# Optimization experiments

Measured on AMD Instinct MI355X. Metric: run time of the kernel, lower is better.

The kernel has to match this reference:

```python
import jax, jax.numpy as jnp
import numpy as np


def setup_inputs() -> dict:
    key = jax.random.key(0)
    k1, k2, k3 = jax.random.split(key, 3)
    B, S, H = 32, 2048, 1024
    lstm_output = jax.random.normal(k1, (B, S, H), dtype=jnp.float32)
    final_hidden = jax.random.normal(k2, (B, H), dtype=jnp.float32)
    # nn.Linear(2H, 1): weight [1, 2H], bias [1]
    W = jax.random.normal(k3, (1, 2 * H), dtype=jnp.float32) * (1.0 / np.sqrt(2 * H))
    b = jnp.zeros((1,), dtype=jnp.float32)
    return {"lstm_output": lstm_output, "final_hidden": final_hidden, "W": W, "b": b}


def reference(lstm_output, final_hidden, W, b):
    # Equivalent to cat([lstm_output, repeat(final_hidden)]) @ W.T + b,
    # but split W to avoid materializing the [B, S, 2H] concat.
    H = lstm_output.shape[-1]
    w1 = W[0, :H]   # applies to lstm_output
    w2 = W[0, H:]   # applies to final_hidden
    # scores: [B, S]
    scores = jnp.einsum('bsh,h->bs', lstm_output, w1) \
           + (final_hidden @ w2)[:, None] + b[0]
    attn_weights = jax.nn.softmax(scores, axis=1)              # [B, S]
    context_vector = jnp.einsum('bs,bsh->bh', attn_weights, lstm_output)
    return context_vector, attn_weights
```

## Files before the change

### kernel.cpp

```cpp
#include <hip/hip_runtime.h>


#define B_ 32
#define S_ 2048
#define H_ 1024
#define ROWS 32
#define WAVES_PER_BATCH (S_ / ROWS)
#define NWAVE (B_ * WAVES_PER_BATCH)
#define NBLK (NWAVE / 4)

__global__ __launch_bounds__(256) void fused_pass(
    const float* __restrict__ lstm, const float* __restrict__ W,
    float* __restrict__ scores, float* __restrict__ part, float* __restrict__ lpart)
{
    const int tid  = threadIdx.x;
    const int wave = tid >> 6;
    const int lane = tid & 63;
    const int gw   = blockIdx.x * 4 + wave;
    const int b    = gw >> 6;
    const int s0   = (gw & 63) * ROWS;

    float4 w[4];
#pragma unroll
    for (int q = 0; q < 4; ++q)
        w[q] = *(const float4*)(W + q * 256 + lane * 4);

    float4 acc[4];
#pragma unroll
    for (int q = 0; q < 4; ++q) acc[q] = make_float4(0.f, 0.f, 0.f, 0.f);
    float l = 0.f;

    const float* base = lstm + ((size_t)b * S_ + s0) * H_ + lane * 4;

    float4 v[4];
#pragma unroll
    for (int q = 0; q < 4; ++q) v[q] = *(const float4*)(base + q * 256);

#pragma unroll
    for (int r = 0; r < ROWS; ++r) {
        float4 nv[4];
        if (r + 1 < ROWS) {
            const float* nb = base + (size_t)(r + 1) * H_;
#pragma unroll
            for (int q = 0; q < 4; ++q) nv[q] = *(const float4*)(nb + q * 256);
        }
        float d = v[0].x * w[0].x + v[0].y * w[0].y + v[0].z * w[0].z + v[0].w * w[0].w;
#pragma unroll
        for (int q = 1; q < 4; ++q)
            d += v[q].x * w[q].x + v[q].y * w[q].y + v[q].z * w[q].z + v[q].w * w[q].w;
#pragma unroll
        for (int off = 32; off >= 1; off >>= 1)
            d += __shfl_xor(d, off, 64);
        if (lane == 0) scores[(size_t)b * S_ + s0 + r] = d;
        const float e = __expf(d);
        l += e;
#pragma unroll
        for (int q = 0; q < 4; ++q) {
            acc[q].x += e * v[q].x; acc[q].y += e * v[q].y;
            acc[q].z += e * v[q].z; acc[q].w += e * v[q].w;
        }
        if (r + 1 < ROWS) {
#pragma unroll
            for (int q = 0; q < 4; ++q) v[q] = nv[q];
        }
    }

    float* pp = part + (size_t)gw * H_ + lane * 4;
#pragma unroll
    for (int q = 0; q < 4; ++q) *(float4*)(pp + q * 256) = acc[q];
    if (lane == 0) lpart[gw] = l;
}

__global__ __launch_bounds__(128) void combine_k(
    const float* __restrict__ part, const float* __restrict__ lpart,
    float* __restrict__ ctx_out, float* __restrict__ Lws)
{
    const int b = blockIdx.x;
    const int h = blockIdx.y * 128 + threadIdx.x;
    float L = 0.f;
#pragma unroll
    for (int j = 0; j < WAVES_PER_BATCH; ++j)
        L += lpart[b * WAVES_PER_BATCH + j];
    float sum = 0.f;
#pragma unroll 8
    for (int j = 0; j < WAVES_PER_BATCH; ++j)
        sum += part[(size_t)(b * WAVES_PER_BATCH + j) * H_ + h];
    ctx_out[(size_t)b * H_ + h] = sum / L;
    if (blockIdx.y == 0 && threadIdx.x == 0) Lws[b] = L;
}

__global__ __launch_bounds__(256) void attn_k(
    const float* __restrict__ scores, const float* __restrict__ Lws,
    float* __restrict__ attn_out)
{
    const int i = blockIdx.x * 256 + threadIdx.x;
    const int b = i >> 9;
    const float invL = 1.0f / Lws[b];
    const float4 sc = ((const float4*)scores)[i];
    float4 o;
    o.x = __expf(sc.x) * invL;
    o.y = __expf(sc.y) * invL;
    o.z = __expf(sc.z) * invL;
    o.w = __expf(sc.w) * invL;
    ((float4*)attn_out)[i] = o;
}

extern "C" void kernel_launch(void* const* d_in, const int* in_sizes, int n_in,
                              void* d_out, int out_size, void* d_ws, size_t ws_size,
                              hipStream_t stream)
{
    const float* lstm = (const float*)d_in[0];
    const float* W    = (const float*)d_in[2];

    float* out  = (float*)d_out;
    float* ctx  = out;
    float* attn = out + B_ * H_;

    float* ws     = (float*)d_ws;
    float* scores = ws;
    float* part   = ws + (size_t)B_ * S_;
    float* lpart  = part + (size_t)NWAVE * H_;
    float* Lws    = lpart + NWAVE;

    fused_pass<<<NBLK, 256, 0, stream>>>(lstm, W, scores, part, lpart);
    combine_k<<<dim3(B_, H_ / 128), 128, 0, stream>>>(part, lpart, ctx, Lws);
    attn_k<<<(B_ * S_) / (4 * 256), 256, 0, stream>>>(scores, Lws, attn);
}
```

Baseline: 403.8 us.

## Batch four-row loads per wave, halve rows per wave, store exp scores

The main pass now loads four rows of lstm_output at once and does their dot products, shuffle reductions and accumulation together. Before, each wave kept only one row of loads in flight ahead of the compute. The number of rows per wave drops from 32 to 16, which doubles the wave count, and exp(score) is written directly so attn_k only has to scale it. The aim is more outstanding memory requests to hide load latency, at the cost of a partial-sum buffer twice as large that combine_k must write and read. combine_k also moves to 256-thread blocks.

```diff
diff --git a/kernel.cpp b/kernel.cpp
--- a/kernel.cpp
+++ b/kernel.cpp
@@ -4,21 +4,21 @@
 #define B_ 32
 #define S_ 2048
 #define H_ 1024
-#define ROWS 32
+#define ROWS 16
 #define WAVES_PER_BATCH (S_ / ROWS)
 #define NWAVE (B_ * WAVES_PER_BATCH)
 #define NBLK (NWAVE / 4)
 
 __global__ __launch_bounds__(256) void fused_pass(
     const float* __restrict__ lstm, const float* __restrict__ W,
-    float* __restrict__ scores, float* __restrict__ part, float* __restrict__ lpart)
+    float* __restrict__ esc, float* __restrict__ part, float* __restrict__ lpart)
 {
     const int tid  = threadIdx.x;
     const int wave = tid >> 6;
     const int lane = tid & 63;
     const int gw   = blockIdx.x * 4 + wave;
-    const int b    = gw >> 6;
-    const int s0   = (gw & 63) * ROWS;
+    const int b    = gw >> 7;
+    const int s0   = (gw & 127) * ROWS;
 
     float4 w[4];
 #pragma unroll
@@ -32,36 +32,49 @@
 
     const float* base = lstm + ((size_t)b * S_ + s0) * H_ + lane * 4;
 
-    float4 v[4];
 #pragma unroll
-    for (int q = 0; q < 4; ++q) v[q] = *(const float4*)(base + q * 256);
+    for (int t = 0; t < ROWS / 4; ++t) {
+        const float* rb = base + (size_t)(t * 4) * H_;
+        float4 v[4][4];
+#pragma unroll
+        for (int r = 0; r < 4; ++r)
+#pragma unroll
+            for (int q = 0; q < 4; ++q)
+                v[r][q] = *(const float4*)(rb + (size_t)r * H_ + q * 256);
 
+        float d[4];
 #pragma unroll
-    for (int r = 0; r < ROWS; ++r) {
-        float4 nv[4];
-        if (r + 1 < ROWS) {
-            const float* nb = base + (size_t)(r + 1) * H_;
+        for (int r = 0; r < 4; ++r) {
+            float s = v[r][0].x * w[0].x + v[r][0].y * w[0].y
+                    + v[r][0].z * w[0].z + v[r][0].w * w[0].w;
 #pragma unroll
-            for (int q = 0; q < 4; ++q) nv[q] = *(const float4*)(nb + q * 256);
+            for (int q = 1; q < 4; ++q)
+                s += v[r][q].x * w[q].x + v[r][q].y * w[q].y
+                   + v[r][q].z * w[q].z + v[r][q].w * w[q].w;
+            d[r] = s;
         }
-        float d = v[0].x * w[0].x + v[0].y * w[0].y + v[0].z * w[0].z + v[0].w * w[0].w;
 #pragma unroll
-        for (int q = 1; q < 4; ++q)
-            d += v[q].x * w[q].x + v[q].y * w[q].y + v[q].z * w[q].z + v[q].w * w[q].w;
+        for (int off = 32; off >= 1; off >>= 1) {
 #pragma unroll
-        for (int off = 32; off >= 1; off >>= 1)
-            d += __shfl_xor(d, off, 64);
-        if (lane == 0) scores[(size_t)b * S_ + s0 + r] = d;
-        const float e = __expf(d);
-        l += e;
+            for (int r = 0; r < 4; ++r)
+                d[r] += __shfl_xor(d[r], off, 64);
+        }
+        float e[4];
 #pragma unroll
-        for (int q = 0; q < 4; ++q) {
-            acc[q].x += e * v[q].x; acc[q].y += e * v[q].y;
-            acc[q].z += e * v[q].z; acc[q].w += e * v[q].w;
-        }
-        if (r + 1 < ROWS) {
+        for (int r = 0; r < 4; ++r) e[r] = __expf(d[r]);
+        if (lane == 0)
+            *(float4*)(esc + (size_t)b * S_ + s0 + t * 4) =
+                make_float4(e[0], e[1], e[2], e[3]);
+        l += (e[0] + e[1]) + (e[2] + e[3]);
 #pragma unroll
-            for (int q = 0; q < 4; ++q) v[q] = nv[q];
+        for (int r = 0; r < 4; ++r) {
+#pragma unroll
+            for (int q = 0; q < 4; ++q) {
+                acc[q].x = fmaf(e[r], v[r][q].x, acc[q].x);
+                acc[q].y = fmaf(e[r], v[r][q].y, acc[q].y);
+                acc[q].z = fmaf(e[r], v[r][q].z, acc[q].z);
+                acc[q].w = fmaf(e[r], v[r][q].w, acc[q].w);
+            }
         }
     }
 
@@ -71,14 +84,14 @@
     if (lane == 0) lpart[gw] = l;
 }
 
-__global__ __launch_bounds__(128) void combine_k(
+__global__ __launch_bounds__(256) void combine_k(
     const float* __restrict__ part, const float* __restrict__ lpart,
     float* __restrict__ ctx_out, float* __restrict__ Lws)
 {
     const int b = blockIdx.x;
-    const int h = blockIdx.y * 128 + threadIdx.x;
+    const int h = blockIdx.y * 256 + threadIdx.x;
     float L = 0.f;
-#pragma unroll
+#pragma unroll 16
     for (int j = 0; j < WAVES_PER_BATCH; ++j)
         L += lpart[b * WAVES_PER_BATCH + j];
     float sum = 0.f;
@@ -90,18 +103,15 @@
 }
 
 __global__ __launch_bounds__(256) void attn_k(
-    const float* __restrict__ scores, const float* __restrict__ Lws,
+    const float* __restrict__ esc, const float* __restrict__ Lws,
     float* __restrict__ attn_out)
 {
     const int i = blockIdx.x * 256 + threadIdx.x;
     const int b = i >> 9;
     const float invL = 1.0f / Lws[b];
-    const float4 sc = ((const float4*)scores)[i];
+    const float4 e = ((const float4*)esc)[i];
     float4 o;
-    o.x = __expf(sc.x) * invL;
-    o.y = __expf(sc.y) * invL;
-    o.z = __expf(sc.z) * invL;
-    o.w = __expf(sc.w) * invL;
+    o.x = e.x * invL; o.y = e.y * invL; o.z = e.z * invL; o.w = e.w * invL;
     ((float4*)attn_out)[i] = o;
 }
 
@@ -116,13 +126,13 @@
     float* ctx  = out;
     float* attn = out + B_ * H_;
 
-    float* ws     = (float*)d_ws;
-    float* scores = ws;
-    float* part   = ws + (size_t)B_ * S_;
-    float* lpart  = part + (size_t)NWAVE * H_;
-    float* Lws    = lpart + NWAVE;
+    float* ws    = (float*)d_ws;
+    float* esc   = ws;
+    float* part  = ws + (size_t)B_ * S_;
+    float* lpart = part + (size_t)NWAVE * H_;
+    float* Lws   = lpart + NWAVE;
 
-    fused_pass<<<NBLK, 256, 0, stream>>>(lstm, W, scores, part, lpart);
-    combine_k<<<dim3(B_, H_ / 128), 128, 0, stream>>>(part, lpart, ctx, Lws);
-    attn_k<<<(B_ * S_) / (4 * 256), 256, 0, stream>>>(scores, Lws, attn);
+    fused_pass<<<NBLK, 256, 0, stream>>>(lstm, W, esc, part, lpart);
+    combine_k<<<dim3(B_, H_ / 256), 256, 0, stream>>>(part, lpart, ctx, Lws);
+    attn_k<<<(B_ * S_) / (4 * 256), 256, 0, stream>>>(esc, Lws, attn);
 }
```

New measurement: 372.3 us. -7.8%, faster.
